# Kernel optimization log

Hardware: AMD Instinct MI355X
Metric: run time of the kernel (lower is better)

Reference implementation:

```python
import jax, jax.numpy as jnp
import numpy as np

N_NODES = 100000
N_EDGES = 1600000
LATENT = 64
NODE_DIM = 7
EDGE_DIM = 3
N_PARAMS = 2

def asinh_layer(p, x):
    # learned asinh: a*arcsinh(b*x + c) + d, p = [a, b, c, d]
    return p[0] * jnp.arcsinh(p[1] * x + p[2]) + p[3]

def mlp2(x, w1, b1, w2, b2):
    # ExplicitMLP([L, L]): gelu between layers, none on last
    return jax.nn.gelu(x @ w1 + b1) @ w2 + b2

def agg_stats(x, n):
    # custom_aggregation: [sum, mean, var, max]; mean/var denominators are n_data
    s = jnp.sum(x, axis=0, keepdims=True)
    m = s / n
    v = jnp.sum((x - m) ** 2, axis=0, keepdims=True) / n
    mx = jnp.max(x, axis=0, keepdims=True)
    return jnp.concatenate([s, m, v, mx], axis=-1)

def _forward(nodes, edges, asinh_node, w_en, b_en, asinh_edge, w_ee, b_ee, asinh_glob, w_eg, b_eg, ew1, eb1, ew2, eb2, nw1, nb1, nw2, nb2, gw1, gb1, gw2, gb2, gw3, gb3, senders):
    # decorate_nodes=False -> zero columns 0:4
    nodes = nodes.at[:, 0:4].set(0.0)
    # globals = arcsinh([n_node, n_edge]) as (1, 2)
    glob = jnp.arcsinh(jnp.array([[float(N_NODES), float(N_EDGES)]], dtype=nodes.dtype))
    # GraphMapFeatures embedding: asinh layer + Dense for nodes/edges/globals
    nodes = asinh_layer(asinh_node, nodes) @ w_en + b_en   # (N, L)
    edges = asinh_layer(asinh_edge, edges) @ w_ee + b_ee   # (E, L)
    glob = asinh_layer(asinh_glob, glob) @ w_eg + b_eg     # (1, L)
    # source overwrites receivers with senders
    recv = senders
    # edge update: concat(edges, nodes[senders], nodes[receivers], globals)
    ge = jnp.broadcast_to(glob, (edges.shape[0], glob.shape[-1]))
    e_in = jnp.concatenate([edges, nodes[senders], nodes[recv], ge], axis=-1)  # (E, 4L)
    edges = mlp2(e_in, ew1, eb1, ew2, eb2)                                     # (E, L)
    # node update: sent/received aggregates are identical since recv == senders
    sent = jax.ops.segment_sum(edges, senders, num_segments=N_NODES)           # (N, L)
    gn = jnp.broadcast_to(glob, (nodes.shape[0], glob.shape[-1]))
    n_in = jnp.concatenate([nodes, sent, sent, gn], axis=-1)                   # (N, 4L)
    nodes = mlp2(n_in, nw1, nb1, nw2, nb2)                                     # (N, L)
    # global update: arcsinh of [sum, mean, var, max] over nodes and edges (single graph)
    node_attr = jnp.arcsinh(agg_stats(nodes, float(N_NODES)))                  # (1, 4L)
    edge_attr = jnp.arcsinh(agg_stats(edges, float(N_EDGES)))                  # (1, 4L)
    g_in = jnp.concatenate([node_attr, edge_attr, glob], axis=-1)              # (1, 9L)
    g = jax.nn.gelu(g_in @ gw1 + gb1)
    g = jax.nn.gelu(g @ gw2 + gb2)
    g = g @ gw3 + gb3
    return g.reshape(-1)  # (N_PARAMS,)

def setup_inputs():
    key = jax.random.key(0)
    ks = jax.random.split(key, 16)
    L = LATENT
    def dense(k, fi, fo):
        return jax.random.normal(k, (fi, fo), jnp.float32) / np.float32(np.sqrt(fi))
    z = lambda n: jnp.zeros((n,), jnp.float32)
    asinh0 = jnp.array([1.0, 1.0, 0.0, 0.0], jnp.float32)
    return {
        "nodes": jax.random.normal(ks[0], (N_NODES, NODE_DIM), jnp.float32),
        "edges": jax.random.normal(ks[1], (N_EDGES, EDGE_DIM), jnp.float32),
        "senders": jax.random.randint(ks[2], (N_EDGES,), 0, N_NODES),
        "asinh_node": asinh0, "w_en": dense(ks[3], NODE_DIM, L), "b_en": z(L),
        "asinh_edge": asinh0, "w_ee": dense(ks[4], EDGE_DIM, L), "b_ee": z(L),
        "asinh_glob": asinh0, "w_eg": dense(ks[5], 2, L), "b_eg": z(L),
        "ew1": dense(ks[6], 4 * L, L), "eb1": z(L),
        "ew2": dense(ks[7], L, L), "eb2": z(L),
        "nw1": dense(ks[8], 4 * L, L), "nb1": z(L),
        "nw2": dense(ks[9], L, L), "nb2": z(L),
        "gw1": dense(ks[10], 9 * L, L), "gb1": z(L),
        "gw2": dense(ks[11], L, L), "gb2": z(L),
        "gw3": dense(ks[12], L, N_PARAMS), "gb3": z(N_PARAMS),
    }

def reference(nodes, edges, senders, asinh_node, w_en, b_en, asinh_edge, w_ee, b_ee, asinh_glob, w_eg, b_eg, ew1, eb1, ew2, eb2, nw1, nb1, nw2, nb2, gw1, gb1, gw2, gb2, gw3, gb3):
    return _forward(nodes, edges, asinh_node, w_en, b_en, asinh_edge, w_ee, b_ee, asinh_glob, w_eg, b_eg, ew1, eb1, ew2, eb2, nw1, nb1, nw2, nb2, gw1, gb1, gw2, gb2, gw3, gb3, senders)
```

## Files before the change

kernel.cpp:

```cpp
#include <hip/hip_runtime.h>
#include <cstdint>
#include <cstddef>

#define NN 100000
#define NE 1600000
#define NSLICE 16
#define NBLK 782

#define PRE_GLOB 0
#define PRE_WC   64
#define PRE_CVEC 256
#define PRE_CN   320
#define PRE_NGV  384
#define PRE_WSR  448
#define PRE_NSR  4544

#define TAB_W2  0
#define TAB_NW1 1
#define TAB_NSR 2
#define TAB_NW2 3
#define TAB_WSR 4

typedef short v8s __attribute__((ext_vector_type(8)));
typedef float v4f __attribute__((ext_vector_type(4)));

__device__ __forceinline__ float asinhf_fast(float x){
    float ax = fabsf(x);
    float r = __logf(ax + sqrtf(fmaf(ax, ax, 1.0f)));
    return copysignf(r, x);
}
__device__ __forceinline__ float gelu_f(float x){
    float x3 = x * x * x;
    float y = 1.5957691216057308f * fmaf(0.044715f, x3, x);
    float e = __expf(y);
    float r = __builtin_amdgcn_rcpf(e + 1.0f);
    return fmaf(-x, r, x);
}
__device__ __forceinline__ unsigned fkey(float f){
    unsigned u = __float_as_uint(f);
    return (u & 0x80000000u) ? ~u : (u | 0x80000000u);
}
__device__ __forceinline__ float funkey(unsigned k){
    unsigned u = (k & 0x80000000u) ? (k ^ 0x80000000u) : ~k;
    return __uint_as_float(u);
}
__device__ __forceinline__ void atomAddF(float* p, float v){
#if defined(__HIP_DEVICE_COMPILE__)
    unsafeAtomicAdd(p, v);
#else
    atomicAdd(p, v);
#endif
}
__device__ __forceinline__ void split8(const float* x, v8s& hi, v8s& lo){
#pragma unroll
    for (int j = 0; j < 8; ++j){
        unsigned u = __float_as_uint(x[j]);
        float hf = __uint_as_float(u & 0xFFFF0000u);
        float r = x[j] - hf;
        hi[j] = (short)(u >> 16);
        lo[j] = (short)(__float_as_uint(r) >> 16);
    }
}
__device__ __forceinline__ v4f mfma3(v8s ah, v8s al, v8s bh, v8s bl, v4f acc){
    acc = __builtin_amdgcn_mfma_f32_16x16x32_bf16(al, bh, acc, 0, 0, 0);
    acc = __builtin_amdgcn_mfma_f32_16x16x32_bf16(ah, bl, acc, 0, 0, 0);
    acc = __builtin_amdgcn_mfma_f32_16x16x32_bf16(ah, bh, acc, 0, 0, 0);
    return acc;
}
__device__ __forceinline__ void fma16(float acc[4][4], float4 a, float4 b){
    float av[4] = {a.x, a.y, a.z, a.w};
    float bv[4] = {b.x, b.y, b.z, b.w};
#pragma unroll
    for (int i = 0; i < 4; ++i)
#pragma unroll
        for (int c = 0; c < 4; ++c)
            acc[i][c] = fmaf(av[i], bv[c], acc[i][c]);
}

__global__ __launch_bounds__(256) void k_pre(const float* an, const float* w_en, const float* b_en,
                      const float* ae, const float* w_ee, const float* b_ee,
                      const float* ag, const float* w_eg, const float* b_eg,
                      const float* ew1, const float* eb1,
                      const float* nw1, const float* nb1,
                      const float* ew2, const float* nw2,
                      float* pre, unsigned short* preB, int* statsZero, int* counts)
{
    __shared__ float gls[64];
    __shared__ float red[3][4][64];
    __shared__ float redc[4][64], redn[4][64];
    int t = threadIdx.x, col = t & 63, qd = t >> 6;
    for (int i = t; i < 2 * NSLICE * 192; i += 256) statsZero[i] = 0;
    {
        int4* c4 = (int4*)counts;
        int4 z = make_int4(0, 0, 0, 0);
        for (int i = t; i < NN / 4; i += 256) c4[i] = z;
    }
    for (int i = t; i < 4096; i += 256){
        pre[PRE_WSR + i] = ew1[4096 + i] + ew1[8192 + i];
        pre[PRE_NSR + i] = nw1[4096 + i] + nw1[8192 + i];
    }
    if (t < 64){
        float g0 = asinhf_fast(100000.0f);
        float g1 = asinhf_fast(1600000.0f);
        float tg0 = fmaf(ag[0], asinhf_fast(fmaf(ag[1], g0, ag[2])), ag[3]);
        float tg1 = fmaf(ag[0], asinhf_fast(fmaf(ag[1], g1, ag[2])), ag[3]);
        float gl = fmaf(tg0, w_eg[t], fmaf(tg1, w_eg[64 + t], b_eg[t]));
        pre[PRE_GLOB + t] = gl;
        gls[t] = gl;
        float tz = fmaf(an[0], asinhf_fast(an[2]), an[3]);
        pre[PRE_CN + t] = fmaf(tz, w_en[t] + w_en[64 + t] + w_en[128 + t] + w_en[192 + t], b_en[t]);
    }
    __syncthreads();
    {
        float s0 = 0.f, s1 = 0.f, s2 = 0.f, sc = 0.f, sn = 0.f;
        int jb = qd * 16;
#pragma unroll 4
        for (int j = jb; j < jb + 16; ++j){
            float e1 = ew1[j * 64 + col];
            s0 = fmaf(w_ee[j], e1, s0);
            s1 = fmaf(w_ee[64 + j], e1, s1);
            s2 = fmaf(w_ee[128 + j], e1, s2);
            sc = fmaf(b_ee[j], e1, sc);
            float g = gls[j];
            sc = fmaf(g, ew1[(192 + j) * 64 + col], sc);
            sn = fmaf(g, nw1[(192 + j) * 64 + col], sn);
        }
        red[0][qd][col] = s0; red[1][qd][col] = s1; red[2][qd][col] = s2;
        redc[qd][col] = sc; redn[qd][col] = sn;
    }
    __syncthreads();
    if (t < 64){
#pragma unroll
        for (int i = 0; i < 3; ++i)
            pre[PRE_WC + i * 64 + t] = (red[i][0][t] + red[i][1][t]) + (red[i][2][t] + red[i][3][t]);
        pre[PRE_CVEC + t] = eb1[t] + (redc[0][t] + redc[1][t]) + (redc[2][t] + redc[3][t]);
        pre[PRE_NGV + t] = nb1[t] + (redn[0][t] + redn[1][t]) + (redn[2][t] + redn[3][t]);
    }
    __syncthreads();
    const float* srcs[5] = {ew2, nw1, pre + PRE_NSR, nw2, pre + PRE_WSR};
    for (int idx = t; idx < 5 * 4096; idx += 256){
        int tab = idx >> 12;
        int rem = idx & 4095;
        int c = rem >> 10;
        int ch = (rem >> 9) & 1;
        int lane = (rem >> 3) & 63;
        int j = rem & 7;
        int k = ch * 32 + (lane >> 4) * 8 + j;
        int n = c * 16 + (lane & 15);
        float v = srcs[tab][k * 64 + n];
        unsigned u = __float_as_uint(v);
        float hf = __uint_as_float(u & 0xFFFF0000u);
        float r = v - hf;
        int base = tab * 8192 + ((c * 2 + ch) * 2) * 512 + lane * 8 + j;
        preB[base] = (unsigned short)(u >> 16);
        preB[base + 512] = (unsigned short)(__float_as_uint(r) >> 16);
    }
}

__global__ __launch_bounds__(256) void k_nproj(const float* nodes, const float* an,
                                               const float* w_en, const float* pre,
                                               const unsigned short* preB,
                                               const int* senders, int* counts,
                                               float* lat, float* nproj)
{
    __shared__ float fz[64][4];
    __shared__ float latS[64][68];
    int t = threadIdx.x;
    int base = blockIdx.x * 64;
    int cnt = NN - base; if (cnt > 64) cnt = 64;
    {
        const int NT = 1563 * 256;
        for (int i = blockIdx.x * 256 + t; i < NE; i += NT)
            atomicAdd(&counts[senders[i]], 1);
    }
    if (t < 64){
        float pa = an[0], pb = an[1], pc = an[2], pd = an[3];
        int n = base + t;
        float t4 = 0.f, t5 = 0.f, t6 = 0.f;
        if (t < cnt){
            const float* row = nodes + (size_t)n * 7;
            t4 = fmaf(pa, asinhf_fast(fmaf(pb, row[4], pc)), pd);
            t5 = fmaf(pa, asinhf_fast(fmaf(pb, row[5], pc)), pd);
            t6 = fmaf(pa, asinhf_fast(fmaf(pb, row[6], pc)), pd);
        }
        fz[t][0] = t4; fz[t][1] = t5; fz[t][2] = t6;
    }
    __syncthreads();
    {
        int k = t & 63, grp = t >> 6;
        float w4 = w_en[4 * 64 + k], w5 = w_en[5 * 64 + k], w6 = w_en[6 * 64 + k];
        float cn = pre[PRE_CN + k];
#pragma unroll
        for (int i = 0; i < 16; ++i){
            int nl = grp * 16 + i;
            float v = 0.f;
            if (nl < cnt){
                v = cn;
                v = fmaf(fz[nl][0], w4, v);
                v = fmaf(fz[nl][1], w5, v);
                v = fmaf(fz[nl][2], w6, v);
                lat[(size_t)(base + nl) * 64 + k] = v;
            }
            latS[nl][k] = v;
        }
    }
    __syncthreads();
    int l = t & 63, w = t >> 6;
    int m = l & 15, q = l >> 4;
    v8s ah[2], al[2];
#pragma unroll
    for (int ch = 0; ch < 2; ++ch){
        float a[8];
        const float* src = &latS[w * 16 + m][ch * 32 + q * 8];
#pragma unroll
        for (int j = 0; j < 8; ++j) a[j] = src[j];
        split8(a, ah[ch], al[ch]);
    }
    const v8s* WB = (const v8s*)(preB + TAB_WSR * 8192);
    v4f acc[4];
#pragma unroll
    for (int c = 0; c < 4; ++c){
        acc[c] = (v4f){0.f, 0.f, 0.f, 0.f};
#pragma unroll
        for (int ch = 0; ch < 2; ++ch){
            v8s bh = WB[((c * 2 + ch) * 2 + 0) * 64 + l];
            v8s bl = WB[((c * 2 + ch) * 2 + 1) * 64 + l];
            acc[c] = mfma3(ah[ch], al[ch], bh, bl, acc[c]);
        }
    }
#pragma unroll
    for (int c = 0; c < 4; ++c)
#pragma unroll
        for (int r = 0; r < 4; ++r){
            int nl = w * 16 + q * 4 + r;
            if (nl < cnt)
                nproj[(size_t)(base + nl) * 64 + c * 16 + m] = acc[c][r];
        }
}

__global__ __launch_bounds__(128) void k_scanA(const int* counts, int* cursor, int* bsums)
{
    __shared__ int sA[128];
    int t = threadIdx.x, b = blockIdx.x;
    int i = b * 128 + t;
    int v = (i < NN) ? counts[i] : 0;
    sA[t] = v;
    __syncthreads();
    for (int off = 1; off < 128; off <<= 1){
        int x = (t >= off) ? sA[t - off] : 0;
        __syncthreads();
        sA[t] += x;
        __syncthreads();
    }
    if (i < NN) cursor[i] = sA[t] - v;
    if (t == 127) bsums[b] = sA[127];
}

__global__ __launch_bounds__(1024) void k_scanB(const int* bsums, int* bpre)
{
    __shared__ int sB[1024];
    int t = threadIdx.x;
    int v = (t < NBLK) ? bsums[t] : 0;
    sB[t] = v;
    __syncthreads();
    for (int off = 1; off < 1024; off <<= 1){
        int x = (t >= off) ? sB[t - off] : 0;
        __syncthreads();
        sB[t] += x;
        __syncthreads();
    }
    if (t < NBLK) bpre[t] = sB[t] - v;
}

__global__ __launch_bounds__(256) void k_assign(const int* senders, int* cursor,
                                                const int* bpre, int* perm)
{
    int i = blockIdx.x * 256 + threadIdx.x;
    int s = senders[i];
    int slot = atomicAdd(&cursor[s], 1) + bpre[s >> 7];
    perm[slot] = i;
}

__global__ __launch_bounds__(256) void k_edge_sorted(const int* perm, const int* senders,
                                                     const float* edges, const float* nproj,
                                                     const float* pre, const unsigned short* preB,
                                                     const float* ae, const float* eb2,
                                                     float* sent, float* epart)
{
    __shared__ float oS[64][65];
    __shared__ float cWs[256];
    __shared__ int sArr[64];
    int t = threadIdx.x;
    cWs[t] = (t < 64) ? pre[PRE_CVEC + t] : pre[PRE_WC + t - 64];
    int l = t & 63, w = t >> 6;
    int m = l & 15, q = l >> 4;
    int e = w * 16 + m;
    int idx = perm[blockIdx.x * 64 + e];
    int s = senders[idx];
    if (q == 0) sArr[e] = s;
    const float* er = edges + (size_t)idx * 3;
    float f0 = er[0], f1 = er[1], f2 = er[2];
    const float4* npb = (const float4*)(nproj + (size_t)s * 64);
    float4 npv0 = npb[2 * q], npv1 = npb[2 * q + 1];
    float4 npv2 = npb[8 + 2 * q], npv3 = npb[8 + 2 * q + 1];
    float pa = ae[0], pb = ae[1], pc = ae[2], pd = ae[3];
    float t0 = fmaf(pa, asinhf_fast(fmaf(pb, f0, pc)), pd);
    float t1 = fmaf(pa, asinhf_fast(fmaf(pb, f1, pc)), pd);
    float t2 = fmaf(pa, asinhf_fast(fmaf(pb, f2, pc)), pd);
    __syncthreads();
    float npf[2][8] = {{npv0.x, npv0.y, npv0.z, npv0.w, npv1.x, npv1.y, npv1.z, npv1.w},
                       {npv2.x, npv2.y, npv2.z, npv2.w, npv3.x, npv3.y, npv3.z, npv3.w}};
    v8s ah[2], al[2];
#pragma unroll
    for (int ch = 0; ch < 2; ++ch){
        int k0 = ch * 32 + q * 8;
        float h[8];
#pragma unroll
        for (int j = 0; j < 8; ++j){
            int k = k0 + j;
            float hp = cWs[k] + npf[ch][j];
            hp = fmaf(t0, cWs[64 + k], hp);
            hp = fmaf(t1, cWs[128 + k], hp);
            hp = fmaf(t2, cWs[192 + k], hp);
            h[j] = gelu_f(hp);
        }
        split8(h, ah[ch], al[ch]);
    }
    const v8s* WB = (const v8s*)(preB + TAB_W2 * 8192);
#pragma unroll
    for (int c = 0; c < 4; ++c){
        v4f acc = (v4f){0.f, 0.f, 0.f, 0.f};
#pragma unroll
        for (int ch = 0; ch < 2; ++ch){
            v8s bh = WB[((c * 2 + ch) * 2 + 0) * 64 + l];
            v8s bl = WB[((c * 2 + ch) * 2 + 1) * 64 + l];
            acc = mfma3(ah[ch], al[ch], bh, bl, acc);
        }
        float bb = eb2[c * 16 + m];
#pragma unroll
        for (int r = 0; r < 4; ++r)
            oS[w * 16 + q * 4 + r][c * 16 + m] = acc[r] + bb;
    }
    __syncthreads();
    if (w == 0){
        int k = l;
        int cur = sArr[0];
        int jstart = 0;
        float a = 0.f;
        for (int j = 0; j < 64; ++j){
            int sj = sArr[j];
            if (sj != cur){
                float* dst = sent + (size_t)cur * 64 + k;
                if (jstart > 0) *dst = a; else atomAddF(dst, a);
                cur = sj; a = 0.f; jstart = j;
            }
            a += oS[j][k];
        }
        atomAddF(sent + (size_t)cur * 64 + k, a);
    } else if (w == 1){
        int k = l;
        float ssum = 0.f, qsum = 0.f, mmax = -INFINITY;
#pragma unroll 4
        for (int j = 0; j < 64; ++j){
            float v = oS[j][k];
            ssum += v;
            qsum = fmaf(v, v, qsum);
            mmax = fmaxf(mmax, v);
        }
        float* ep = epart + (size_t)(blockIdx.x & (NSLICE - 1)) * 192;
        atomAddF(ep + k, ssum);
        atomAddF(ep + 64 + k, qsum);
        atomicMax((unsigned*)(ep + 128) + k, fkey(mmax));
    }
}

__global__ __launch_bounds__(256) void k_edge_atomic(const float* edges, const int* senders,
                                                     const float* nproj, const float* pre,
                                                     const float* ae, const float* ew2, const float* eb2,
                                                     float* sent, float* epart)
{
    __shared__ float hT[64][68];
    __shared__ int sArr[64];
    int t = threadIdx.x;
    int e = t & 63, kq = t >> 6;
    int eg = blockIdx.x * 64 + e;
    int s = senders[eg];
    if (kq == 0) sArr[e] = s;
    float pa = ae[0], pb = ae[1], pc = ae[2], pd = ae[3];
    const float* erow = edges + (size_t)eg * 3;
    float t0 = fmaf(pa, asinhf_fast(fmaf(pb, erow[0], pc)), pd);
    float t1 = fmaf(pa, asinhf_fast(fmaf(pb, erow[1], pc)), pd);
    float t2 = fmaf(pa, asinhf_fast(fmaf(pb, erow[2], pc)), pd);
    int j0 = kq * 16;
    const float* np = nproj + (size_t)s * 64 + j0;
    float npv[16];
#pragma unroll
    for (int qq = 0; qq < 4; ++qq){
        float4 v = *(const float4*)(np + qq * 4);
        npv[qq * 4 + 0] = v.x; npv[qq * 4 + 1] = v.y; npv[qq * 4 + 2] = v.z; npv[qq * 4 + 3] = v.w;
    }
    const float* Wc = pre + PRE_WC;
    const float* cvec = pre + PRE_CVEC;
#pragma unroll
    for (int jj = 0; jj < 16; ++jj){
        int j = j0 + jj;
        float hp = cvec[j] + npv[jj];
        hp = fmaf(t0, Wc[j], hp);
        hp = fmaf(t1, Wc[64 + j], hp);
        hp = fmaf(t2, Wc[128 + j], hp);
        hT[j][e] = gelu_f(hp);
    }
    __syncthreads();
    int e0 = (t & 15) * 4, k0 = (t >> 4) * 4;
    float acc[4][4];
    {
        float4 bb = *(const float4*)(eb2 + k0);
#pragma unroll
        for (int i = 0; i < 4; ++i){ acc[i][0] = bb.x; acc[i][1] = bb.y; acc[i][2] = bb.z; acc[i][3] = bb.w; }
    }
#pragma unroll 4
    for (int j = 0; j < 64; ++j){
        float4 a = *(const float4*)&hT[j][e0];
        float4 b = *(const float4*)(ew2 + j * 64 + k0);
        fma16(acc, a, b);
    }
#pragma unroll
    for (int i = 0; i < 4; ++i){
        int sv = sArr[e0 + i];
        float* dst = sent + (size_t)sv * 64 + k0;
        atomAddF(dst + 0, acc[i][0]);
        atomAddF(dst + 1, acc[i][1]);
        atomAddF(dst + 2, acc[i][2]);
        atomAddF(dst + 3, acc[i][3]);
    }
    float ps[4], pq[4], pm[4];
#pragma unroll
    for (int c = 0; c < 4; ++c){
        float s0 = acc[0][c], s1 = acc[1][c], s2 = acc[2][c], s3 = acc[3][c];
        ps[c] = (s0 + s1) + (s2 + s3);
        pq[c] = fmaf(s0, s0, fmaf(s1, s1, fmaf(s2, s2, s3 * s3)));
        pm[c] = fmaxf(fmaxf(s0, s1), fmaxf(s2, s3));
    }
#pragma unroll
    for (int msk = 1; msk < 16; msk <<= 1){
#pragma unroll
        for (int c = 0; c < 4; ++c){
            ps[c] += __shfl_xor(ps[c], msk);
            pq[c] += __shfl_xor(pq[c], msk);
            pm[c] = fmaxf(pm[c], __shfl_xor(pm[c], msk));
        }
    }
    float* ep = epart + (size_t)(blockIdx.x & (NSLICE - 1)) * 192;
    if ((t & 15) == 0){
#pragma unroll
        for (int c = 0; c < 4; ++c){
            atomAddF(ep + k0 + c, ps[c]);
            atomAddF(ep + 64 + k0 + c, pq[c]);
            atomicMax((unsigned*)(ep + 128) + k0 + c, fkey(pm[c]));
        }
    }
}

__global__ __launch_bounds__(256) void k_node(const float* lat, const float* sent, const float* pre,
                                              const unsigned short* preB, const float* nb2,
                                              float* npart)
{
    __shared__ float h2S[64][68];
    __shared__ float sS[4][64], qS[4][64], mS[4][64];
    int t = threadIdx.x;
    int base = blockIdx.x * 64;
    int cnt = NN - base; if (cnt > 64) cnt = 64;
    int l = t & 63, w = t >> 6;
    int m = l & 15, q = l >> 4;
    int rowA = w * 16 + m;
    bool vA = rowA < cnt;
    v8s lh[2], ll[2], sh[2], sl[2];
#pragma unroll
    for (int ch = 0; ch < 2; ++ch){
        float a[8] = {0,0,0,0,0,0,0,0}, b[8] = {0,0,0,0,0,0,0,0};
        if (vA){
            const float4* pl = (const float4*)(lat + (size_t)(base + rowA) * 64 + ch * 32 + q * 8);
            const float4* psn = (const float4*)(sent + (size_t)(base + rowA) * 64 + ch * 32 + q * 8);
            float4 a0 = pl[0], a1 = pl[1], b0 = psn[0], b1 = psn[1];
            a[0]=a0.x; a[1]=a0.y; a[2]=a0.z; a[3]=a0.w; a[4]=a1.x; a[5]=a1.y; a[6]=a1.z; a[7]=a1.w;
            b[0]=b0.x; b[1]=b0.y; b[2]=b0.z; b[3]=b0.w; b[4]=b1.x; b[5]=b1.y; b[6]=b1.z; b[7]=b1.w;
        }
        split8(a, lh[ch], ll[ch]);
        split8(b, sh[ch], sl[ch]);
    }
    const v8s* B1 = (const v8s*)(preB + TAB_NW1 * 8192);
    const v8s* BS = (const v8s*)(preB + TAB_NSR * 8192);
    v4f acc[4];
#pragma unroll
    for (int c = 0; c < 4; ++c){
        acc[c] = (v4f){0.f, 0.f, 0.f, 0.f};
#pragma unroll
        for (int ch = 0; ch < 2; ++ch){
            v8s bh = B1[((c * 2 + ch) * 2 + 0) * 64 + l];
            v8s bl = B1[((c * 2 + ch) * 2 + 1) * 64 + l];
            acc[c] = mfma3(lh[ch], ll[ch], bh, bl, acc[c]);
            v8s ch2 = BS[((c * 2 + ch) * 2 + 0) * 64 + l];
            v8s cl2 = BS[((c * 2 + ch) * 2 + 1) * 64 + l];
            acc[c] = mfma3(sh[ch], sl[ch], ch2, cl2, acc[c]);
        }
        float g = pre[PRE_NGV + c * 16 + m];
#pragma unroll
        for (int r = 0; r < 4; ++r)
            h2S[w * 16 + q * 4 + r][c * 16 + m] = gelu_f(acc[c][r] + g);
    }
    __syncthreads();
    v8s ah[2], al[2];
#pragma unroll
    for (int ch = 0; ch < 2; ++ch){
        float a[8];
        const float* src = &h2S[w * 16 + m][ch * 32 + q * 8];
#pragma unroll
        for (int j = 0; j < 8; ++j) a[j] = src[j];
        split8(a, ah[ch], al[ch]);
    }
    const v8s* B2 = (const v8s*)(preB + TAB_NW2 * 8192);
    float ps[4], pq[4], pm[4];
#pragma unroll
    for (int c = 0; c < 4; ++c){
        v4f a2 = (v4f){0.f, 0.f, 0.f, 0.f};
#pragma unroll
        for (int ch = 0; ch < 2; ++ch){
            v8s bh = B2[((c * 2 + ch) * 2 + 0) * 64 + l];
            v8s bl = B2[((c * 2 + ch) * 2 + 1) * 64 + l];
            a2 = mfma3(ah[ch], al[ch], bh, bl, a2);
        }
        float bb = nb2[c * 16 + m];
        ps[c] = 0.f; pq[c] = 0.f; pm[c] = -INFINITY;
#pragma unroll
        for (int r = 0; r < 4; ++r){
            int nl = w * 16 + q * 4 + r;
            if (nl < cnt){
                float v = a2[r] + bb;
                ps[c] += v;
                pq[c] = fmaf(v, v, pq[c]);
                pm[c] = fmaxf(pm[c], v);
            }
        }
    }
#pragma unroll
    for (int msk = 16; msk <= 32; msk <<= 1){
#pragma unroll
        for (int c = 0; c < 4; ++c){
            ps[c] += __shfl_xor(ps[c], msk);
            pq[c] += __shfl_xor(pq[c], msk);
            pm[c] = fmaxf(pm[c], __shfl_xor(pm[c], msk));
        }
    }
    if (l < 16){
#pragma unroll
        for (int c = 0; c < 4; ++c){
            sS[w][c * 16 + l] = ps[c];
            qS[w][c * 16 + l] = pq[c];
            mS[w][c * 16 + l] = pm[c];
        }
    }
    __syncthreads();
    if (t < 64){
        int k = t;
        float ssum = sS[0][k] + sS[1][k] + sS[2][k] + sS[3][k];
        float qsum = qS[0][k] + qS[1][k] + qS[2][k] + qS[3][k];
        float mmax = fmaxf(fmaxf(mS[0][k], mS[1][k]), fmaxf(mS[2][k], mS[3][k]));
        float* np = npart + (size_t)(blockIdx.x & (NSLICE - 1)) * 192;
        atomAddF(np + k, ssum);
        atomAddF(np + 64 + k, qsum);
        atomicMax((unsigned*)(np + 128) + k, fkey(mmax));
    }
}

__global__ __launch_bounds__(256) void k_final(const float* pre, const float* epart, const float* npart,
                        const float* gw1, const float* gb1, const float* gw2, const float* gb2,
                        const float* gw3, const float* gb3, float* out)
{
    __shared__ float gin[576];
    __shared__ float p1[4][64];
    __shared__ float l1s[64];
    __shared__ float l2s[64];
    int t = threadIdx.x;
    if (t < 64){
        float ns = 0.f, nq = 0.f; unsigned nmk = 0u;
        float es = 0.f, eq = 0.f; unsigned emk = 0u;
        for (int sl = 0; sl < NSLICE; ++sl){
            const float* np = npart + (size_t)sl * 192;
            const float* ep = epart + (size_t)sl * 192;
            ns += np[t]; nq += np[64 + t];
            unsigned a = ((const unsigned*)(np + 128))[t]; if (a > nmk) nmk = a;
            es += ep[t]; eq += ep[64 + t];
            unsigned b = ((const unsigned*)(ep + 128))[t]; if (b > emk) emk = b;
        }
        float mean = ns / 100000.0f;
        float var = nq / 100000.0f - mean * mean;
        gin[t] = asinhf_fast(ns);
        gin[64 + t] = asinhf_fast(mean);
        gin[128 + t] = asinhf_fast(var);
        gin[192 + t] = asinhf_fast(funkey(nmk));
        float meane = es / 1600000.0f;
        float vare = eq / 1600000.0f - meane * meane;
        gin[256 + t] = asinhf_fast(es);
        gin[320 + t] = asinhf_fast(meane);
        gin[384 + t] = asinhf_fast(vare);
        gin[448 + t] = asinhf_fast(funkey(emk));
        gin[512 + t] = pre[PRE_GLOB + t];
    }
    __syncthreads();
    {
        int col = t & 63, qq = t >> 6;
        float a1 = 0.f;
        for (int j = qq * 144; j < qq * 144 + 144; ++j)
            a1 = fmaf(gin[j], gw1[j * 64 + col], a1);
        p1[qq][col] = a1;
    }
    __syncthreads();
    if (t < 64){
        float a = gb1[t] + ((p1[0][t] + p1[1][t]) + (p1[2][t] + p1[3][t]));
        l1s[t] = gelu_f(a);
    }
    __syncthreads();
    if (t < 64){
        float a2 = gb2[t];
        for (int j = 0; j < 64; ++j) a2 = fmaf(l1s[j], gw2[j * 64 + t], a2);
        l2s[t] = gelu_f(a2);
    }
    __syncthreads();
    if (t < 2){
        float s = gb3[t];
        for (int j = 0; j < 64; ++j) s = fmaf(l2s[j], gw3[j * 2 + t], s);
        out[t] = s;
    }
}

extern "C" void kernel_launch(void* const* d_in, const int* in_sizes, int n_in,
                              void* d_out, int out_size, void* d_ws, size_t ws_size,
                              hipStream_t stream)
{
    const float* nodes  = (const float*)d_in[0];
    const float* edges  = (const float*)d_in[1];
    const int*   senders= (const int*)d_in[2];
    const float* an  = (const float*)d_in[3];
    const float* w_en= (const float*)d_in[4];
    const float* b_en= (const float*)d_in[5];
    const float* ae  = (const float*)d_in[6];
    const float* w_ee= (const float*)d_in[7];
    const float* b_ee= (const float*)d_in[8];
    const float* ag  = (const float*)d_in[9];
    const float* w_eg= (const float*)d_in[10];
    const float* b_eg= (const float*)d_in[11];
    const float* ew1 = (const float*)d_in[12];
    const float* eb1 = (const float*)d_in[13];
    const float* ew2 = (const float*)d_in[14];
    const float* eb2 = (const float*)d_in[15];
    const float* nw1 = (const float*)d_in[16];
    const float* nb1 = (const float*)d_in[17];
    const float* nw2 = (const float*)d_in[18];
    const float* nb2 = (const float*)d_in[19];
    const float* gw1 = (const float*)d_in[20];
    const float* gb1 = (const float*)d_in[21];
    const float* gw2 = (const float*)d_in[22];
    const float* gb2 = (const float*)d_in[23];
    const float* gw3 = (const float*)d_in[24];
    const float* gb3 = (const float*)d_in[25];

    char* ws = (char*)d_ws;
    float*  lat   = (float*)(ws);
    float*  nproj = (float*)(ws + 25600000);
    float*  sent  = (float*)(ws + 51200000);
    float*  pre   = (float*)(ws + 76800000);
    unsigned short* preB = (unsigned short*)(ws + 76865536);
    float*  epart = (float*)(ws + 76963840);
    float*  npart = (float*)(ws + 76976128);
    int*    counts= (int*)  (ws + 77000000);
    int*    cursor= (int*)  (ws + 77400000);
    int*    bsums = (int*)  (ws + 77800000);
    int*    bpre  = (int*)  (ws + 77804096);
    int*    perm  = (int*)  (ws + 77810000);

    const size_t NEED_FAST = 84210000;
    bool fast = (ws_size >= NEED_FAST);

    hipMemsetAsync(sent, 0, (size_t)NN * 64 * sizeof(float), stream);

    hipLaunchKernelGGL(k_pre, dim3(1), dim3(256), 0, stream,
                       an, w_en, b_en, ae, w_ee, b_ee, ag, w_eg, b_eg, ew1, eb1,
                       nw1, nb1, ew2, nw2, pre, preB, (int*)epart, counts);

    if (fast){
        hipLaunchKernelGGL(k_nproj, dim3((NN + 63) / 64), dim3(256), 0, stream,
                           nodes, an, w_en, pre, preB, senders, counts, lat, nproj);
        hipLaunchKernelGGL(k_scanA, dim3(NBLK), dim3(128), 0, stream, counts, cursor, bsums);
        hipLaunchKernelGGL(k_scanB, dim3(1), dim3(1024), 0, stream, bsums, bpre);
        hipLaunchKernelGGL(k_assign, dim3(NE / 256), dim3(256), 0, stream,
                           senders, cursor, bpre, perm);
        hipLaunchKernelGGL(k_edge_sorted, dim3(NE / 64), dim3(256), 0, stream,
                           perm, senders, edges, nproj, pre, preB, ae, eb2, sent, epart);
    } else {
        hipLaunchKernelGGL(k_nproj, dim3((NN + 63) / 64), dim3(256), 0, stream,
                           nodes, an, w_en, pre, preB, senders, cursor, lat, nproj);
        hipLaunchKernelGGL(k_edge_atomic, dim3(NE / 64), dim3(256), 0, stream,
                           edges, senders, nproj, pre, ae, ew2, eb2, sent, epart);
    }

    hipLaunchKernelGGL(k_node, dim3((NN + 63) / 64), dim3(256), 0, stream,
                       lat, sent, pre, preB, nb2, npart);
    hipLaunchKernelGGL(k_final, dim3(1), dim3(256), 0, stream,
                       pre, epart, npart, gw1, gb1, gw2, gb2, gw3, gb3, (float*)d_out);
}
```

Before: 516.2 us.

## Replace global-atomic edge permutation with two-pass bucketed counting sort

The single k_assign kernel, which did a global atomicAdd per edge on per-node cursors and scattered edge indices into perm, is replaced by a two-level bucket sort. k_binA bins each chunk of edges into 256-node buckets using shared-memory histograms and writes them contiguously per bucket. k_binB then places each bucket's edges into their final sorted positions with shared-memory atomics and staging, so the writes to perm are coalesced. The aim is to cut global atomic contention and random scatter, at the cost of an extra kernel launch, an extra pass over the indices, and more workspace.

```diff
diff --git a/kernel.cpp b/kernel.cpp
--- a/kernel.cpp
+++ b/kernel.cpp
@@ -6,6 +6,9 @@
 #define NE 1600000
 #define NSLICE 16
 #define NBLK 782
+#define NBUCK 391
+#define CHA 4096
+#define CAPB 6144
 
 #define PRE_GLOB 0
 #define PRE_WC   64
@@ -256,7 +259,7 @@
     if (t == 127) bsums[b] = sA[127];
 }
 
-__global__ __launch_bounds__(1024) void k_scanB(const int* bsums, int* bpre)
+__global__ __launch_bounds__(1024) void k_scanB(const int* bsums, int* bpre, int* bucketFill)
 {
     __shared__ int sB[1024];
     int t = threadIdx.x;
@@ -270,15 +273,86 @@
         __syncthreads();
     }
     if (t < NBLK) bpre[t] = sB[t] - v;
-}
-
-__global__ __launch_bounds__(256) void k_assign(const int* senders, int* cursor,
-                                                const int* bpre, int* perm)
-{
-    int i = blockIdx.x * 256 + threadIdx.x;
-    int s = senders[i];
-    int slot = atomicAdd(&cursor[s], 1) + bpre[s >> 7];
-    perm[slot] = i;
+    if (t < NBUCK) bucketFill[t] = (t == 0) ? 0 : sB[2 * t - 1];
+}
+
+__global__ __launch_bounds__(256) void k_binA(const int* senders, int* bucketFill, int* binned)
+{
+    __shared__ int hist[NBUCK], hist2[NBUCK], runS[NBUCK];
+    __shared__ int lofs[NBUCK + 1];
+    __shared__ int sA[512];
+    __shared__ int staged[CHA];
+    int t = threadIdx.x, b = blockIdx.x;
+    int beg = b * CHA;
+    int end = beg + CHA; if (end > NE) end = NE;
+    int n = end - beg;
+    for (int i = t; i < NBUCK; i += 256){ hist[i] = 0; hist2[i] = 0; }
+    __syncthreads();
+    for (int i = beg + t; i < end; i += 256)
+        atomicAdd(&hist[senders[i] >> 8], 1);
+    __syncthreads();
+    sA[t] = (t < NBUCK) ? hist[t] : 0;
+    sA[t + 256] = (t + 256 < NBUCK) ? hist[t + 256] : 0;
+    __syncthreads();
+    for (int off = 1; off < 512; off <<= 1){
+        int x0 = (t >= off) ? sA[t - off] : 0;
+        int p = t + 256;
+        int x1 = (p >= off) ? sA[p - off] : 0;
+        __syncthreads();
+        sA[t] += x0; sA[p] += x1;
+        __syncthreads();
+    }
+    if (t < NBUCK) lofs[t] = sA[t] - hist[t];
+    if (t + 256 < NBUCK) lofs[t + 256] = sA[t + 256] - hist[t + 256];
+    if (t == 0) lofs[NBUCK] = n;
+    for (int i = t; i < NBUCK; i += 256)
+        if (hist[i] > 0) runS[i] = atomicAdd(&bucketFill[i], hist[i]);
+    __syncthreads();
+    for (int i = beg + t; i < end; i += 256){
+        int bk = senders[i] >> 8;
+        int r = atomicAdd(&hist2[bk], 1);
+        staged[lofs[bk] + r] = i;
+    }
+    __syncthreads();
+    for (int p = t; p < n; p += 256){
+        int lo = 0, hi = NBUCK;
+        while (hi - lo > 1){
+            int mid = (lo + hi) >> 1;
+            if (lofs[mid] <= p) lo = mid; else hi = mid;
+        }
+        binned[runS[lo] + (p - lofs[lo])] = staged[p];
+    }
+}
+
+__global__ __launch_bounds__(256) void k_binB(const int* binned, const int* senders,
+                                              const int* cursor, const int* bpre, int* perm)
+{
+    __shared__ int cnt256[256];
+    __shared__ int staged[CAPB];
+    int t = threadIdx.x, b = blockIdx.x;
+    int base = bpre[2 * b];
+    int end = (b == NBUCK - 1) ? NE : bpre[2 * b + 2];
+    int cnt = end - base;
+    cnt256[t] = 0;
+    __syncthreads();
+    if (cnt <= CAPB){
+        for (int i = base + t; i < end; i += 256){
+            int idx = binned[i];
+            int s = senders[idx];
+            int r = atomicAdd(&cnt256[s & 255], 1);
+            int pos = cursor[s] + bpre[s >> 7] + r;
+            staged[pos - base] = idx;
+        }
+        __syncthreads();
+        for (int i = t; i < cnt; i += 256) perm[base + i] = staged[i];
+    } else {
+        for (int i = base + t; i < end; i += 256){
+            int idx = binned[i];
+            int s = senders[idx];
+            int r = atomicAdd(&cnt256[s & 255], 1);
+            perm[cursor[s] + bpre[s >> 7] + r] = idx;
+        }
+    }
 }
 
 __global__ __launch_bounds__(256) void k_edge_sorted(const int* perm, const int* senders,
@@ -677,8 +751,10 @@
     int*    bsums = (int*)  (ws + 77800000);
     int*    bpre  = (int*)  (ws + 77804096);
     int*    perm  = (int*)  (ws + 77810000);
-
-    const size_t NEED_FAST = 84210000;
+    int*    binned= (int*)  (ws + 84210000);
+    int*    bucketFill = (int*)(ws + 90610000);
+
+    const size_t NEED_FAST = 90620000;
     bool fast = (ws_size >= NEED_FAST);
 
     hipMemsetAsync(sent, 0, (size_t)NN * 64 * sizeof(float), stream);
@@ -691,9 +767,10 @@
         hipLaunchKernelGGL(k_nproj, dim3((NN + 63) / 64), dim3(256), 0, stream,
                            nodes, an, w_en, pre, preB, senders, counts, lat, nproj);
         hipLaunchKernelGGL(k_scanA, dim3(NBLK), dim3(128), 0, stream, counts, cursor, bsums);
-        hipLaunchKernelGGL(k_scanB, dim3(1), dim3(1024), 0, stream, bsums, bpre);
-        hipLaunchKernelGGL(k_assign, dim3(NE / 256), dim3(256), 0, stream,
-                           senders, cursor, bpre, perm);
+        hipLaunchKernelGGL(k_scanB, dim3(1), dim3(1024), 0, stream, bsums, bpre, bucketFill);
+        hipLaunchKernelGGL(k_binA, dim3(NBUCK), dim3(256), 0, stream, senders, bucketFill, binned);
+        hipLaunchKernelGGL(k_binB, dim3(NBUCK), dim3(256), 0, stream,
+                           binned, senders, cursor, bpre, perm);
         hipLaunchKernelGGL(k_edge_sorted, dim3(NE / 64), dim3(256), 0, stream,
                            perm, senders, edges, nproj, pre, preB, ae, eb2, sent, epart);
     } else {
```

Measured after the change: 437.2 us. 15.3% less time.
